# Optimization experiments

Hardware: AMD Instinct MI355X
Metric: run time of the kernel (lower is better)

The kernel has to match this reference:

```python
import jax, jax.numpy as jnp
import numpy as np

N = 50000      # nodes
E = 800000     # edges
G = 32         # graphs in batch
C = 10         # num_classes


def _glorot(key, shape):
    lim = float(np.sqrt(6.0 / (shape[0] + shape[1])))
    return jax.random.uniform(key, shape, jnp.float32, -lim, lim)


def setup_inputs() -> dict:
    key = jax.random.key(0)
    ks = jax.random.split(key, 10)
    norm = jax.random.normal(ks[0], (N, 3), jnp.float32)
    pos = jax.random.normal(ks[1], (N, 3), jnp.float32)
    x = jax.random.normal(ks[2], (N, 2), jnp.float32)
    edge_index = jax.random.randint(ks[3], (2, E), 0, N, dtype=jnp.int64)
    batch = jnp.sort(jax.random.randint(ks[4], (N,), 0, G, dtype=jnp.int64))
    return {
        'norm': norm, 'pos': pos, 'x': x,
        'edge_index': edge_index, 'batch': batch,
        'W1': _glorot(ks[5], (8, 64)),   'b1': jnp.zeros((64,), jnp.float32),
        'W2': _glorot(ks[6], (72, 128)), 'b2': jnp.zeros((128,), jnp.float32),
        'W3': _glorot(ks[7], (208, 256)),'b3': jnp.zeros((256,), jnp.float32),
        'Wl': _glorot(ks[8], (256, C)),  'bl': jnp.zeros((C,), jnp.float32),
    }


def gcn_conv(h, W, b, src, dst):
    # GCNConv(normalize=False), edge_weight == 1: out_i = sum_{(j->i)} (h_j @ W) + b
    m = h @ W                      # [N, F_out] dense transform first (cheaper than per-edge)
    msg = m[src]                   # gather per edge [E, F_out]
    agg = jax.ops.segment_sum(msg, dst, num_segments=N)
    return agg + b


def reference(norm, pos, x, edge_index, batch, W1, b1, W2, b2, W3, b3, Wl, bl):
    inp = jnp.concatenate([norm, pos, x], axis=1)      # [N, 8]
    src, dst = edge_index[0], edge_index[1]
    # dropout p=0.2 is identity at inference
    h1 = jax.nn.relu(gcn_conv(inp, W1, b1, src, dst))  # [N, 64]
    h = jnp.concatenate([h1, inp], axis=1)             # [N, 72]
    h2 = jax.nn.relu(gcn_conv(h, W2, b2, src, dst))    # [N, 128]
    h = jnp.concatenate([h, h2, inp], axis=1)          # [N, 208]
    h3 = jax.nn.relu(gcn_conv(h, W3, b3, src, dst))    # [N, 256]
    pooled = jax.ops.segment_max(h3, batch, num_segments=G)  # global_max_pool [G, 256]
    logits = pooled @ Wl + bl
    out = jax.nn.log_softmax(logits, axis=1)
    pred = jax.nn.softmax(out, axis=1)
    return (out, pred)
```

## Files before the change

kernel.cpp:

```cpp
#include <hip/hip_runtime.h>
#include <hip/hip_bf16.h>

#define NN 50000
#define EE 800000
#define GG 32
#define SCB 512

#define BSH 6
#define NBUK 782
#define NBLK1 256
#define EPB (EE / NBLK1)
#define MH (NBUK * NBLK1)
#define NB2 ((MH + SCB - 1) / SCB)
#define CAP2 2048

#define B_PREP ((NN + 255) / 256)
#define TOTW (64 * 32 + 128 * 96 + 256 * 224)
#define B_WTP ((TOTW + 255) / 256)

using short8 = __attribute__((ext_vector_type(8))) short;
using f32x4  = __attribute__((ext_vector_type(4))) float;

__device__ __forceinline__ ushort f2bf(float f) {
    __hip_bfloat16 hb = __float2bfloat16(f);
    return *reinterpret_cast<ushort*>(&hb);
}

__device__ __forceinline__ void acc8(uint4 v, float* a) {
    a[0] += __uint_as_float(v.x << 16); a[1] += __uint_as_float(v.x & 0xffff0000u);
    a[2] += __uint_as_float(v.y << 16); a[3] += __uint_as_float(v.y & 0xffff0000u);
    a[4] += __uint_as_float(v.z << 16); a[5] += __uint_as_float(v.z & 0xffff0000u);
    a[6] += __uint_as_float(v.w << 16); a[7] += __uint_as_float(v.w & 0xffff0000u);
}

__device__ __forceinline__ void wtp_one(const float* W, ushort* Wt, int K, int F,
                                        int KPAD, int mode, int idx) {
    int n = idx / KPAD, k = idx - n * KPAD;
    float v = 0.f;
    if (k < K) {
        int ko = k;
        if (mode == 2) ko = (k < 8) ? (k + 64) : (k - 8);
        v = W[(size_t)ko * F + n];
        if (mode == 1 && ko >= 64 && ko < 72) v += W[(size_t)(ko + 136) * F + n];
    }
    Wt[idx] = f2bf(v);
}


__global__ __launch_bounds__(256) void setup_k(
        const int* __restrict__ edst, int* __restrict__ hist,
        const float* __restrict__ nrm, const float* __restrict__ pos,
        const float* __restrict__ x, ushort* __restrict__ inpb,
        const float* __restrict__ W1, ushort* __restrict__ Wt1,
        const float* __restrict__ W2, ushort* __restrict__ Wt2,
        const float* __restrict__ W3, ushort* __restrict__ Wt3,
        float* __restrict__ pooled) {
    int blk = blockIdx.x, tid = threadIdx.x;
    if (blk < NBLK1) {
        __shared__ uint cnt[NBUK];
        for (int i = tid; i < NBUK; i += 256) cnt[i] = 0;
        __syncthreads();
        int base = blk * EPB;
        for (int i = tid; i < EPB; i += 256)
            atomicAdd(&cnt[(uint)edst[base + i] >> BSH], 1u);
        __syncthreads();
        for (int b = tid; b < NBUK; b += 256)
            hist[(size_t)b * NBLK1 + blk] = (int)cnt[b];
    } else if (blk < NBLK1 + B_PREP) {
        int i = (blk - NBLK1) * 256 + tid;
        if (i < NN) {
            float v[8];
            v[0] = nrm[i * 3]; v[1] = nrm[i * 3 + 1]; v[2] = nrm[i * 3 + 2];
            v[3] = pos[i * 3]; v[4] = pos[i * 3 + 1]; v[5] = pos[i * 3 + 2];
            v[6] = x[i * 2];   v[7] = x[i * 2 + 1];
            uint4 d;
            d.x = (uint)f2bf(v[0]) | ((uint)f2bf(v[1]) << 16);
            d.y = (uint)f2bf(v[2]) | ((uint)f2bf(v[3]) << 16);
            d.z = (uint)f2bf(v[4]) | ((uint)f2bf(v[5]) << 16);
            d.w = (uint)f2bf(v[6]) | ((uint)f2bf(v[7]) << 16);
            *reinterpret_cast<uint4*>(&inpb[(size_t)i * 8]) = d;
        }
    } else if (blk < NBLK1 + B_PREP + B_WTP) {
        int idx = (blk - NBLK1 - B_PREP) * 256 + tid;
        if (idx < 64 * 32) { wtp_one(W1, Wt1, 8, 64, 32, 0, idx); return; }
        idx -= 64 * 32;
        if (idx < 128 * 96) { wtp_one(W2, Wt2, 72, 128, 96, 2, idx); return; }
        idx -= 128 * 96;
        if (idx < 256 * 224) wtp_one(W3, Wt3, 200, 256, 224, 1, idx);
    } else {
        for (int q = tid; q < GG * 256; q += 256) pooled[q] = 0.f;
    }
}


__global__ __launch_bounds__(SCB) void scan1_k(const int* __restrict__ in,
                                               int* __restrict__ bsum, int M) {
    __shared__ int ws[SCB / 64];
    int tid = threadIdx.x, lane = tid & 63, w = tid >> 6;
    int i = blockIdx.x * SCB + tid;
    int s = (i < M) ? in[i] : 0;
    #pragma unroll
    for (int off = 32; off >= 1; off >>= 1) s += __shfl_down(s, off, 64);
    if (lane == 0) ws[w] = s;
    __syncthreads();
    if (tid == 0) {
        int t = 0;
        #pragma unroll
        for (int j = 0; j < SCB / 64; j++) t += ws[j];
        bsum[blockIdx.x] = t;
    }
}

__global__ __launch_bounds__(64) void scan2g_k(int* __restrict__ bsum, int nb) {
    int lane = threadIdx.x;
    int carry = 0;
    for (int base = 0; base < nb; base += 64) {
        int v = (base + lane < nb) ? bsum[base + lane] : 0;
        int s = v;
        #pragma unroll
        for (int off = 1; off < 64; off <<= 1) {
            int t = __shfl_up(s, off, 64);
            if (lane >= off) s += t;
        }
        if (base + lane < nb) bsum[base + lane] = carry + s - v;
        carry += __shfl(s, 63, 64);
    }
}

__global__ __launch_bounds__(SCB) void scan3g_k(const int* __restrict__ in,
                                                const int* __restrict__ bsum,
                                                int* __restrict__ out, int M) {
    __shared__ int ws[SCB / 64];
    int tid = threadIdx.x, lane = tid & 63, w = tid >> 6;
    int i = blockIdx.x * SCB + tid;
    int v = (i < M) ? in[i] : 0;
    int s = v;
    #pragma unroll
    for (int off = 1; off < 64; off <<= 1) {
        int t = __shfl_up(s, off, 64);
        if (lane >= off) s += t;
    }
    if (lane == 63) ws[w] = s;
    __syncthreads();
    if (w == 0 && lane < SCB / 64) {
        int t = ws[lane];
        #pragma unroll
        for (int off = 1; off < SCB / 64; off <<= 1) {
            int u = __shfl_up(t, off, 64);
            if (lane >= off) t += u;
        }
        ws[lane] = t;
    }
    __syncthreads();
    if (i < M) out[i] = (w ? ws[w - 1] : 0) + s - v + bsum[blockIdx.x];
}


__global__ __launch_bounds__(256) void bsort1_k(const int* __restrict__ esrc,
                                                const int* __restrict__ edst,
                                                const int* __restrict__ ofs,
                                                uint* __restrict__ packed) {
    __shared__ uint cnt[1024];
    __shared__ uint lofs0[1024];
    __shared__ uint goff[NBUK];
    __shared__ uint stage[EPB];
    __shared__ uint wsum[4];
    int tid = threadIdx.x, blk = blockIdx.x;
    int lane = tid & 63, wv = tid >> 6;

    for (int i = tid; i < 1024; i += 256) cnt[i] = 0;
    __syncthreads();
    int base = blk * EPB;
    for (int i = tid; i < EPB; i += 256)
        atomicAdd(&cnt[(uint)edst[base + i] >> BSH], 1u);
    __syncthreads();

    uint c0 = cnt[tid * 4 + 0], c1 = cnt[tid * 4 + 1];
    uint c2 = cnt[tid * 4 + 2], c3 = cnt[tid * 4 + 3];
    uint ts = c0 + c1 + c2 + c3;
    uint sc = ts;
    #pragma unroll
    for (int off = 1; off < 64; off <<= 1) {
        uint t = __shfl_up(sc, off, 64);
        if (lane >= off) sc += t;
    }
    if (lane == 63) wsum[wv] = sc;
    __syncthreads();
    uint wbase = 0;
    for (int j = 0; j < wv; j++) wbase += wsum[j];
    uint run = wbase + sc - ts;
    lofs0[tid * 4 + 0] = run;
    lofs0[tid * 4 + 1] = run + c0;
    lofs0[tid * 4 + 2] = run + c0 + c1;
    lofs0[tid * 4 + 3] = run + c0 + c1 + c2;
    cnt[tid * 4 + 0] = run;
    cnt[tid * 4 + 1] = run + c0;
    cnt[tid * 4 + 2] = run + c0 + c1;
    cnt[tid * 4 + 3] = run + c0 + c1 + c2;
    for (int b = tid; b < NBUK; b += 256)
        goff[b] = (uint)ofs[(size_t)b * NBLK1 + blk];
    __syncthreads();

    for (int i = tid; i < EPB; i += 256) {
        int d = edst[base + i];
        uint b = (uint)d >> BSH;
        uint pos = atomicAdd(&cnt[b], 1u);
        stage[pos] = (b << 22) | ((uint)(d & 63) << 16) | (uint)esrc[base + i];
    }
    __syncthreads();

    for (int i = tid; i < EPB; i += 256) {
        uint p = stage[i];
        uint b = p >> 22;
        packed[goff[b] + ((uint)i - lofs0[b])] = p & 0x3FFFFFu;
    }
}


__global__ __launch_bounds__(256) void bsort2_k(const uint* __restrict__ packed,
                                                const int* __restrict__ ofs,
                                                ushort* __restrict__ col,
                                                int* __restrict__ rowptr) {
    __shared__ uint buf[CAP2];
    __shared__ ushort srt[CAP2];
    __shared__ uint fcnt[64], fofs[64];
    int b = blockIdx.x, tid = threadIdx.x;
    uint g0 = (uint)ofs[(size_t)b * NBLK1];
    uint g1 = (b + 1 < NBUK) ? (uint)ofs[(size_t)(b + 1) * NBLK1] : (uint)EE;
    uint n = g1 - g0;
    if (tid < 64) fcnt[tid] = 0;
    __syncthreads();
    for (uint i = tid; i < n; i += 256) {
        uint p = packed[g0 + i];
        buf[i] = p;
        atomicAdd(&fcnt[(p >> 16) & 63], 1u);
    }
    __syncthreads();
    if (tid < 64) {
        uint v = fcnt[tid], s = v;
        #pragma unroll
        for (int off = 1; off < 64; off <<= 1) {
            uint t = __shfl_up(s, off, 64);
            if (tid >= off) s += t;
        }
        uint e0 = s - v;
        fofs[tid] = e0;
        int node = (b << BSH) + tid;
        if (node < NN) rowptr[node] = (int)(g0 + e0);
    }
    if (b == NBUK - 1 && tid == 0) rowptr[NN] = EE;
    __syncthreads();
    for (uint i = tid; i < n; i += 256) {
        uint p = buf[i];
        uint pos = atomicAdd(&fofs[(p >> 16) & 63], 1u);
        srt[pos] = (ushort)(p & 0xFFFFu);
    }
    __syncthreads();
    for (uint i = tid; i < n; i += 256) col[g0 + i] = srt[i];
}


template <int K, int KPAD, int LDA, int F, int WPA, int WPB, int WG, bool POOL>
__global__ __launch_bounds__(512) void layer_k(
        const ushort* __restrict__ preA, const ushort* __restrict__ preB,
        const ushort* __restrict__ gsrc,
        const int* __restrict__ rowptr, const ushort* __restrict__ col,
        const ushort* __restrict__ Wt, const float* __restrict__ bias,
        ushort* __restrict__ aggout, ushort* __restrict__ out,
        const int* __restrict__ batch, float* __restrict__ pooled, int N) {
    constexpr int WPRE = WPA + WPB;
    constexpr int NU4 = WG / 8;
    constexpr int TPN = (NU4 < 8) ? NU4 : 8;
    constexpr int U4PT = NU4 / TPN;
    constexpr int KS = KPAD / 32;
    constexpr int FW = F / 4;
    constexpr int NT = FW / 16;

    __shared__ ushort At[64 * LDA];
    __shared__ int batchv[64];

    const int node0 = blockIdx.x * 64;
    const int tid = threadIdx.x;
    const int lane = tid & 63;
    const int wv = tid >> 6;
    const int wm = wv & 1;
    const int wn = wv >> 1;

    {
        int m = tid / TPN;
        int j = tid - m * TPN;
        if (m < 64) {
            int i = node0 + m;
            float ga0[U4PT * 8], ga1[U4PT * 8];
            #pragma unroll
            for (int q = 0; q < U4PT * 8; q++) { ga0[q] = 0.f; ga1[q] = 0.f; }
            if (i < N) {
                int e0 = rowptr[i], e1 = rowptr[i + 1];
                int e = e0;
                for (; e + 1 < e1; e += 2) {
                    int s0 = col[e], s1 = col[e + 1];
                    #pragma unroll
                    for (int u = 0; u < U4PT; u++) {
                        uint4 v0 = *reinterpret_cast<const uint4*>(
                            &gsrc[(size_t)s0 * WG + (j * U4PT + u) * 8]);
                        uint4 v1 = *reinterpret_cast<const uint4*>(
                            &gsrc[(size_t)s1 * WG + (j * U4PT + u) * 8]);
                        acc8(v0, ga0 + u * 8);
                        acc8(v1, ga1 + u * 8);
                    }
                }
                if (e < e1) {
                    int s0 = col[e];
                    #pragma unroll
                    for (int u = 0; u < U4PT; u++) {
                        uint4 v0 = *reinterpret_cast<const uint4*>(
                            &gsrc[(size_t)s0 * WG + (j * U4PT + u) * 8]);
                        acc8(v0, ga0 + u * 8);
                    }
                }
            }
            #pragma unroll
            for (int u = 0; u < U4PT; u++) {
                uint4 o;
                o.x = (uint)f2bf(ga0[u*8+0] + ga1[u*8+0]) | ((uint)f2bf(ga0[u*8+1] + ga1[u*8+1]) << 16);
                o.y = (uint)f2bf(ga0[u*8+2] + ga1[u*8+2]) | ((uint)f2bf(ga0[u*8+3] + ga1[u*8+3]) << 16);
                o.z = (uint)f2bf(ga0[u*8+4] + ga1[u*8+4]) | ((uint)f2bf(ga0[u*8+5] + ga1[u*8+5]) << 16);
                o.w = (uint)f2bf(ga0[u*8+6] + ga1[u*8+6]) | ((uint)f2bf(ga0[u*8+7] + ga1[u*8+7]) << 16);
                *reinterpret_cast<uint4*>(&At[m * LDA + WPRE + (j * U4PT + u) * 8]) = o;
                if (aggout != nullptr && i < N)
                    *reinterpret_cast<uint4*>(&aggout[(size_t)i * WG + (j * U4PT + u) * 8]) = o;
            }
        }
        if constexpr (POOL) {
            if (tid < 64) batchv[tid] = (node0 + tid < N) ? batch[node0 + tid] : -1;
        }
    }

    if constexpr (WPRE > 0) {
        constexpr int NP = WPRE / 8;
        for (int idx = tid; idx < 64 * NP; idx += 512) {
            int m = idx / NP, q = idx - m * NP;
            int i = node0 + m;
            uint4 v = make_uint4(0, 0, 0, 0);
            if (i < N) {
                int c = q * 8;
                if (c < WPA) v = *reinterpret_cast<const uint4*>(&preA[(size_t)i * WPA + c]);
                else v = *reinterpret_cast<const uint4*>(&preB[(size_t)i * WPB + (c - WPA)]);
            }
            *reinterpret_cast<uint4*>(&At[m * LDA + q * 8]) = v;
        }
    }
    {
        constexpr int PADU4 = (KPAD - K) / 8;
        for (int idx = tid; idx < 64 * PADU4; idx += 512) {
            int m = idx / PADU4, q = idx - m * PADU4;
            *reinterpret_cast<uint4*>(&At[m * LDA + K + q * 8]) = make_uint4(0, 0, 0, 0);
        }
    }
    __syncthreads();

    const int r15 = lane & 15, kg = lane >> 4;

    short8 a[2][KS];
    #pragma unroll
    for (int s = 0; s < 2; s++)
        #pragma unroll
        for (int kc = 0; kc < KS; kc++)
            a[s][kc] = *reinterpret_cast<const short8*>(
                &At[(wm * 32 + s * 16 + r15) * LDA + kg * 8 + kc * 32]);

    f32x4 acc[2][NT];
    #pragma unroll
    for (int s = 0; s < 2; s++)
        #pragma unroll
        for (int nt = 0; nt < NT; nt++) acc[s][nt] = (f32x4){0.f, 0.f, 0.f, 0.f};

    const ushort* wbase = &Wt[(size_t)(wn * FW + r15) * KPAD + kg * 8];
    #pragma unroll
    for (int nt = 0; nt < NT; nt++) {
        short8 b[KS];
        #pragma unroll
        for (int kc = 0; kc < KS; kc++)
            b[kc] = *reinterpret_cast<const short8*>(
                wbase + (size_t)nt * 16 * KPAD + kc * 32);
        #pragma unroll
        for (int kc = 0; kc < KS; kc++) {
            acc[0][nt] = __builtin_amdgcn_mfma_f32_16x16x32_bf16(a[0][kc], b[kc], acc[0][nt], 0, 0, 0);
            acc[1][nt] = __builtin_amdgcn_mfma_f32_16x16x32_bf16(a[1][kc], b[kc], acc[1][nt], 0, 0, 0);
        }
    }

    if constexpr (!POOL) {
        #pragma unroll
        for (int s = 0; s < 2; s++)
            #pragma unroll
            for (int nt = 0; nt < NT; nt++) {
                int colg = wn * FW + nt * 16 + r15;
                float bv = bias[colg];
                #pragma unroll
                for (int reg = 0; reg < 4; reg++) {
                    int row = node0 + wm * 32 + s * 16 + kg * 4 + reg;
                    if (row < N) {
                        float v = fmaxf(acc[s][nt][reg] + bv, 0.f);
                        out[(size_t)row * F + colg] = f2bf(v);
                    }
                }
            }
    } else {
        __syncthreads();
        ushort* H3 = At;
        #pragma unroll
        for (int s = 0; s < 2; s++)
            #pragma unroll
            for (int nt = 0; nt < NT; nt++) {
                int colg = wn * FW + nt * 16 + r15;
                float bv = bias[colg];
                #pragma unroll
                for (int reg = 0; reg < 4; reg++) {
                    int m = wm * 32 + s * 16 + kg * 4 + reg;
                    float v = fmaxf(acc[s][nt][reg] + bv, 0.f);
                    H3[m * 256 + colg] = f2bf(v);
                }
            }
        __syncthreads();
        int nvalid = min(64, N - node0);
        int c = tid & 255, half = tid >> 8;
        int m0 = half * 32;
        int m1 = min(m0 + 32, nvalid);
        int curg = -1;
        float cm = 0.f;
        for (int m = m0; m < m1; m++) {
            int g = batchv[m];
            if (g != curg) {
                if (curg >= 0)
                    atomicMax(reinterpret_cast<int*>(&pooled[curg * 256 + c]),
                              __float_as_int(cm));
                curg = g;
                cm = 0.f;
            }
            cm = fmaxf(cm, __uint_as_float((uint)H3[m * 256 + c] << 16));
        }
        if (curg >= 0)
            atomicMax(reinterpret_cast<int*>(&pooled[curg * 256 + c]),
                      __float_as_int(cm));
    }
}


__global__ __launch_bounds__(320) void head_k(const float* __restrict__ pooled,
                                              const float* __restrict__ Wl,
                                              const float* __restrict__ bl,
                                              float* __restrict__ out) {
    __shared__ float lg[GG][10];
    __shared__ float lse[GG];
    int t = threadIdx.x;
    int g = t / 10, c = t % 10;
    float acc = bl[c];
    for (int k = 0; k < 256; k++) acc = fmaf(pooled[g * 256 + k], Wl[k * 10 + c], acc);
    lg[g][c] = acc;
    __syncthreads();
    if (c == 0) {
        float mx = -1e30f;
        for (int j = 0; j < 10; j++) mx = fmaxf(mx, lg[g][j]);
        float s = 0.f;
        for (int j = 0; j < 10; j++) s += expf(lg[g][j] - mx);
        lse[g] = mx + logf(s);
    }
    __syncthreads();
    float o = acc - lse[g];
    out[g * 10 + c] = o;
    out[320 + g * 10 + c] = expf(o);
}


extern "C" void kernel_launch(void* const* d_in, const int* in_sizes, int n_in,
                              void* d_out, int out_size, void* d_ws, size_t ws_size,
                              hipStream_t stream) {
    const int N = NN, E = EE;
    const float* nrm = (const float*)d_in[0];
    const float* pos = (const float*)d_in[1];
    const float* x   = (const float*)d_in[2];
    const int* ei    = (const int*)d_in[3];
    const int* batch = (const int*)d_in[4];
    const float* W1 = (const float*)d_in[5];
    const float* b1 = (const float*)d_in[6];
    const float* W2 = (const float*)d_in[7];
    const float* b2 = (const float*)d_in[8];
    const float* W3 = (const float*)d_in[9];
    const float* b3 = (const float*)d_in[10];
    const float* Wl = (const float*)d_in[11];
    const float* bl = (const float*)d_in[12];

    const int* esrc = ei;
    const int* edst = ei + E;

    char* w = (char*)d_ws;
    auto carve = [&](size_t bytes) {
        void* p = (void*)w;
        w += (bytes + 255) & ~(size_t)255;
        return p;
    };
    int* hist     = (int*)carve((size_t)MH * 4);
    int* ofs      = (int*)carve((size_t)MH * 4);
    int* bsum     = (int*)carve((size_t)NB2 * 4);
    uint* packed  = (uint*)carve((size_t)E * 4);
    int* rowptr   = (int*)carve((size_t)(N + 1) * 4);
    ushort* col   = (ushort*)carve((size_t)E * 2);
    ushort* inpb  = (ushort*)carve((size_t)N * 8 * 2);
    ushort* agg1  = (ushort*)carve((size_t)N * 8 * 2);
    ushort* h1    = (ushort*)carve((size_t)N * 64 * 2);
    ushort* aggh1 = (ushort*)carve((size_t)N * 64 * 2);
    ushort* h2    = (ushort*)carve((size_t)N * 128 * 2);
    ushort* Wt1   = (ushort*)carve((size_t)64 * 32 * 2);
    ushort* Wt2   = (ushort*)carve((size_t)128 * 96 * 2);
    ushort* Wt3   = (ushort*)carve((size_t)256 * 224 * 2);
    float* pooled = (float*)carve((size_t)GG * 256 * 4);

    setup_k<<<NBLK1 + B_PREP + B_WTP + 1, 256, 0, stream>>>(
        edst, hist, nrm, pos, x, inpb, W1, Wt1, W2, Wt2, W3, Wt3, pooled);

    scan1_k<<<NB2, SCB, 0, stream>>>(hist, bsum, MH);
    scan2g_k<<<1, 64, 0, stream>>>(bsum, NB2);
    scan3g_k<<<NB2, SCB, 0, stream>>>(hist, bsum, ofs, MH);
    bsort1_k<<<NBLK1, 256, 0, stream>>>(esrc, edst, ofs, packed);
    bsort2_k<<<NBUK, 256, 0, stream>>>(packed, ofs, col, rowptr);

    layer_k<8, 32, 40, 64, 0, 0, 8, false><<<NBUK, 512, 0, stream>>>(
        nullptr, nullptr, inpb, rowptr, col, Wt1, b1, agg1, h1, nullptr, nullptr, N);

    layer_k<72, 96, 104, 128, 8, 0, 64, false><<<NBUK, 512, 0, stream>>>(
        agg1, nullptr, h1, rowptr, col, Wt2, b2, aggh1, h2, nullptr, nullptr, N);

    layer_k<200, 224, 264, 256, 64, 8, 128, true><<<NBUK, 512, 0, stream>>>(
        aggh1, agg1, h2, rowptr, col, Wt3, b3, nullptr, nullptr, batch, pooled, N);

    head_k<<<1, 320, 0, stream>>>(pooled, Wl, bl, (float*)d_out);
}
```

Before: 138.6 us.

## Balance edge aggregation across block threads with shared-memory atomic accumulation

```diff
diff --git a/kernel.cpp b/kernel.cpp
--- a/kernel.cpp
+++ b/kernel.cpp
@@ -33,15 +33,22 @@
     a[6] += __uint_as_float(v.w << 16); a[7] += __uint_as_float(v.w & 0xffff0000u);
 }
 
+__device__ __forceinline__ short8 pack_bf8(const float* p) {
+    union { ushort u[8]; short8 s; } r;
+    #pragma unroll
+    for (int q = 0; q < 8; q++) r.u[q] = f2bf(p[q]);
+    return r.s;
+}
+
 __device__ __forceinline__ void wtp_one(const float* W, ushort* Wt, int K, int F,
                                         int KPAD, int mode, int idx) {
     int n = idx / KPAD, k = idx - n * KPAD;
     float v = 0.f;
     if (k < K) {
         int ko = k;
-        if (mode == 2) ko = (k < 8) ? (k + 64) : (k - 8);
+        if (mode == 3) ko = (k < 128) ? (k + 72) : (k - 128);
         v = W[(size_t)ko * F + n];
-        if (mode == 1 && ko >= 64 && ko < 72) v += W[(size_t)(ko + 136) * F + n];
+        if (mode == 3 && ko >= 64 && ko < 72) v += W[(size_t)(ko + 136) * F + n];
     }
     Wt[idx] = f2bf(v);
 }
@@ -84,9 +91,9 @@
         int idx = (blk - NBLK1 - B_PREP) * 256 + tid;
         if (idx < 64 * 32) { wtp_one(W1, Wt1, 8, 64, 32, 0, idx); return; }
         idx -= 64 * 32;
-        if (idx < 128 * 96) { wtp_one(W2, Wt2, 72, 128, 96, 2, idx); return; }
+        if (idx < 128 * 96) { wtp_one(W2, Wt2, 72, 128, 96, 0, idx); return; }
         idx -= 128 * 96;
-        if (idx < 256 * 224) wtp_one(W3, Wt3, 200, 256, 224, 1, idx);
+        if (idx < 256 * 224) wtp_one(W3, Wt3, 200, 256, 224, 3, idx);
     } else {
         for (int q = tid; q < GG * 256; q += 256) pooled[q] = 0.f;
     }
@@ -260,7 +267,7 @@
 }
 
 
-template <int K, int KPAD, int LDA, int F, int WPA, int WPB, int WG, bool POOL>
+template <int KPAD, int GR, int WG, int PREW, int WPA, int WPB, int F, bool POOL>
 __global__ __launch_bounds__(512) void layer_k(
         const ushort* __restrict__ preA, const ushort* __restrict__ preB,
         const ushort* __restrict__ gsrc,
@@ -268,15 +275,17 @@
         const ushort* __restrict__ Wt, const float* __restrict__ bias,
         ushort* __restrict__ aggout, ushort* __restrict__ out,
         const int* __restrict__ batch, float* __restrict__ pooled, int N) {
-    constexpr int WPRE = WPA + WPB;
-    constexpr int NU4 = WG / 8;
-    constexpr int TPN = (NU4 < 8) ? NU4 : 8;
-    constexpr int U4PT = NU4 / TPN;
-    constexpr int KS = KPAD / 32;
-    constexpr int FW = F / 4;
-    constexpr int NT = FW / 16;
-
-    __shared__ ushort At[64 * LDA];
+    constexpr int GRP = GR + 4;
+    constexpr int SL  = WG / 8;
+    constexpr int R   = 512 / SL;
+    constexpr int PRS = (PREW > 0) ? PREW + 8 : 8;
+    constexpr int KS  = KPAD / 32;
+    constexpr int FW  = F / 4;
+    constexpr int NT  = FW / 16;
+
+    __shared__ float accA[64 * GRP];
+    __shared__ ushort Atpre[(PREW > 0) ? 64 * PRS : 8];
+    __shared__ int rp[65];
     __shared__ int batchv[64];
 
     const int node0 = blockIdx.x * 64;
@@ -286,58 +295,14 @@
     const int wm = wv & 1;
     const int wn = wv >> 1;
 
-    {
-        int m = tid / TPN;
-        int j = tid - m * TPN;
-        if (m < 64) {
-            int i = node0 + m;
-            float ga0[U4PT * 8], ga1[U4PT * 8];
-            #pragma unroll
-            for (int q = 0; q < U4PT * 8; q++) { ga0[q] = 0.f; ga1[q] = 0.f; }
-            if (i < N) {
-                int e0 = rowptr[i], e1 = rowptr[i + 1];
-                int e = e0;
-                for (; e + 1 < e1; e += 2) {
-                    int s0 = col[e], s1 = col[e + 1];
-                    #pragma unroll
-                    for (int u = 0; u < U4PT; u++) {
-                        uint4 v0 = *reinterpret_cast<const uint4*>(
-                            &gsrc[(size_t)s0 * WG + (j * U4PT + u) * 8]);
-                        uint4 v1 = *reinterpret_cast<const uint4*>(
-                            &gsrc[(size_t)s1 * WG + (j * U4PT + u) * 8]);
-                        acc8(v0, ga0 + u * 8);
-                        acc8(v1, ga1 + u * 8);
-                    }
-                }
-                if (e < e1) {
-                    int s0 = col[e];
-                    #pragma unroll
-                    for (int u = 0; u < U4PT; u++) {
-                        uint4 v0 = *reinterpret_cast<const uint4*>(
-                            &gsrc[(size_t)s0 * WG + (j * U4PT + u) * 8]);
-                        acc8(v0, ga0 + u * 8);
-                    }
-                }
-            }
-            #pragma unroll
-            for (int u = 0; u < U4PT; u++) {
-                uint4 o;
-                o.x = (uint)f2bf(ga0[u*8+0] + ga1[u*8+0]) | ((uint)f2bf(ga0[u*8+1] + ga1[u*8+1]) << 16);
-                o.y = (uint)f2bf(ga0[u*8+2] + ga1[u*8+2]) | ((uint)f2bf(ga0[u*8+3] + ga1[u*8+3]) << 16);
-                o.z = (uint)f2bf(ga0[u*8+4] + ga1[u*8+4]) | ((uint)f2bf(ga0[u*8+5] + ga1[u*8+5]) << 16);
-                o.w = (uint)f2bf(ga0[u*8+6] + ga1[u*8+6]) | ((uint)f2bf(ga0[u*8+7] + ga1[u*8+7]) << 16);
-                *reinterpret_cast<uint4*>(&At[m * LDA + WPRE + (j * U4PT + u) * 8]) = o;
-                if (aggout != nullptr && i < N)
-                    *reinterpret_cast<uint4*>(&aggout[(size_t)i * WG + (j * U4PT + u) * 8]) = o;
-            }
-        }
-        if constexpr (POOL) {
-            if (tid < 64) batchv[tid] = (node0 + tid < N) ? batch[node0 + tid] : -1;
-        }
-    }
-
-    if constexpr (WPRE > 0) {
-        constexpr int NP = WPRE / 8;
+    for (int idx = tid; idx < 64 * GRP / 4; idx += 512)
+        *reinterpret_cast<float4*>(&accA[idx * 4]) = make_float4(0.f, 0.f, 0.f, 0.f);
+    if (tid < 65) rp[tid] = rowptr[min(node0 + tid, NN)];
+    if constexpr (POOL) {
+        if (tid < 64) batchv[tid] = (node0 + tid < N) ? batch[node0 + tid] : -1;
+    }
+    if constexpr (PREW > 0) {
+        constexpr int NP = PREW / 8;
         for (int idx = tid; idx < 64 * NP; idx += 512) {
             int m = idx / NP, q = idx - m * NP;
             int i = node0 + m;
@@ -345,29 +310,90 @@
             if (i < N) {
                 int c = q * 8;
                 if (c < WPA) v = *reinterpret_cast<const uint4*>(&preA[(size_t)i * WPA + c]);
-                else v = *reinterpret_cast<const uint4*>(&preB[(size_t)i * WPB + (c - WPA)]);
-            }
-            *reinterpret_cast<uint4*>(&At[m * LDA + q * 8]) = v;
-        }
-    }
+                else if (c < WPA + WPB) v = *reinterpret_cast<const uint4*>(&preB[(size_t)i * WPB + (c - WPA)]);
+            }
+            *reinterpret_cast<uint4*>(&Atpre[m * PRS + q * 8]) = v;
+        }
+    }
+    __syncthreads();
+
     {
-        constexpr int PADU4 = (KPAD - K) / 8;
-        for (int idx = tid; idx < 64 * PADU4; idx += 512) {
-            int m = idx / PADU4, q = idx - m * PADU4;
-            *reinterpret_cast<uint4*>(&At[m * LDA + K + q * 8]) = make_uint4(0, 0, 0, 0);
-        }
-    }
-    __syncthreads();
+        int e0 = rp[0], e1 = rp[64];
+        int nE = e1 - e0;
+        int j = tid % SL;
+        int r = tid / SL;
+        int per = (nE + R - 1) / R;
+        int es = e0 + r * per;
+        int ee = min(es + per, e1);
+        if (es < ee) {
+            int lo = 0, hi = 63;
+            while (lo < hi) {
+                int mid = (lo + hi + 1) >> 1;
+                if (rp[mid] <= es) lo = mid; else hi = mid - 1;
+            }
+            int m = lo;
+            float a0[8] = {0,0,0,0,0,0,0,0};
+            float a1[8] = {0,0,0,0,0,0,0,0};
+            int e = es;
+            while (true) {
+                int segend = min(rp[m + 1], ee);
+                for (; e + 1 < segend; e += 2) {
+                    int s0 = col[e], s1 = col[e + 1];
+                    uint4 v0 = *reinterpret_cast<const uint4*>(&gsrc[(size_t)s0 * WG + j * 8]);
+                    uint4 v1 = *reinterpret_cast<const uint4*>(&gsrc[(size_t)s1 * WG + j * 8]);
+                    acc8(v0, a0); acc8(v1, a1);
+                }
+                if (e < segend) {
+                    uint4 v0 = *reinterpret_cast<const uint4*>(&gsrc[(size_t)col[e] * WG + j * 8]);
+                    acc8(v0, a0); e++;
+                }
+                float* dst = &accA[m * GRP + j * 8];
+                #pragma unroll
+                for (int q = 0; q < 8; q++) atomicAdd(&dst[q], a0[q] + a1[q]);
+                if (segend >= ee) break;
+                m++;
+                while (rp[m + 1] <= e) m++;
+                #pragma unroll
+                for (int q = 0; q < 8; q++) { a0[q] = 0.f; a1[q] = 0.f; }
+            }
+        }
+    }
+    __syncthreads();
+
+    if (aggout != nullptr) {
+        constexpr int NV = WG / 8;
+        for (int idx = tid; idx < 64 * NV; idx += 512) {
+            int m = idx / NV, q = idx - m * NV;
+            int i = node0 + m;
+            if (i < N) {
+                const float* p = &accA[m * GRP + q * 8];
+                uint4 o;
+                o.x = (uint)f2bf(p[0]) | ((uint)f2bf(p[1]) << 16);
+                o.y = (uint)f2bf(p[2]) | ((uint)f2bf(p[3]) << 16);
+                o.z = (uint)f2bf(p[4]) | ((uint)f2bf(p[5]) << 16);
+                o.w = (uint)f2bf(p[6]) | ((uint)f2bf(p[7]) << 16);
+                *reinterpret_cast<uint4*>(&aggout[(size_t)i * WG + q * 8]) = o;
+            }
+        }
+    }
 
     const int r15 = lane & 15, kg = lane >> 4;
 
     short8 a[2][KS];
     #pragma unroll
-    for (int s = 0; s < 2; s++)
-        #pragma unroll
-        for (int kc = 0; kc < KS; kc++)
-            a[s][kc] = *reinterpret_cast<const short8*>(
-                &At[(wm * 32 + s * 16 + r15) * LDA + kg * 8 + kc * 32]);
+    for (int s = 0; s < 2; s++) {
+        int row = wm * 32 + s * 16 + r15;
+        #pragma unroll
+        for (int kc = 0; kc < KS; kc++) {
+            if (kc * 32 < GR) {
+                const float* p = &accA[row * GRP + kc * 32 + kg * 8];
+                a[s][kc] = pack_bf8(p);
+            } else {
+                a[s][kc] = *reinterpret_cast<const short8*>(
+                    &Atpre[row * PRS + (kc * 32 - GR) + kg * 8]);
+            }
+        }
+    }
 
     f32x4 acc[2][NT];
     #pragma unroll
@@ -408,7 +434,7 @@
             }
     } else {
         __syncthreads();
-        ushort* H3 = At;
+        ushort* H3 = reinterpret_cast<ushort*>(accA);
         #pragma unroll
         for (int s = 0; s < 2; s++)
             #pragma unroll
@@ -525,13 +551,13 @@
     bsort1_k<<<NBLK1, 256, 0, stream>>>(esrc, edst, ofs, packed);
     bsort2_k<<<NBUK, 256, 0, stream>>>(packed, ofs, col, rowptr);
 
-    layer_k<8, 32, 40, 64, 0, 0, 8, false><<<NBUK, 512, 0, stream>>>(
+    layer_k<32, 32, 8, 0, 0, 0, 64, false><<<NBUK, 512, 0, stream>>>(
         nullptr, nullptr, inpb, rowptr, col, Wt1, b1, agg1, h1, nullptr, nullptr, N);
 
-    layer_k<72, 96, 104, 128, 8, 0, 64, false><<<NBUK, 512, 0, stream>>>(
+    layer_k<96, 64, 64, 32, 8, 0, 128, false><<<NBUK, 512, 0, stream>>>(
         agg1, nullptr, h1, rowptr, col, Wt2, b2, aggh1, h2, nullptr, nullptr, N);
 
-    layer_k<200, 224, 264, 256, 64, 8, 128, true><<<NBUK, 512, 0, stream>>>(
+    layer_k<224, 128, 128, 96, 64, 8, 256, true><<<NBUK, 512, 0, stream>>>(
         aggh1, agg1, h2, rowptr, col, Wt3, b3, nullptr, nullptr, batch, pooled, N);
 
     head_k<<<1, 320, 0, stream>>>(pooled, Wl, bl, (float*)d_out);
```

New measurement: 241.8 us. +74.5%, slower.

## Template node tile size; use 32-node blocks in layer 3 with 4-way edge unroll

Applied to the files above, without the earlier changes.

```diff
diff --git a/kernel.cpp b/kernel.cpp
--- a/kernel.cpp
+++ b/kernel.cpp
@@ -13,6 +13,7 @@
 #define MH (NBUK * NBLK1)
 #define NB2 ((MH + SCB - 1) / SCB)
 #define CAP2 2048
+#define NBLK32 1563
 
 #define B_PREP ((NN + 255) / 256)
 #define TOTW (64 * 32 + 128 * 96 + 256 * 224)
@@ -260,7 +261,7 @@
 }
 
 
-template <int K, int KPAD, int LDA, int F, int WPA, int WPB, int WG, bool POOL>
+template <int NODES, int K, int KPAD, int LDA, int F, int WPA, int WPB, int WG, bool POOL>
 __global__ __launch_bounds__(512) void layer_k(
         const ushort* __restrict__ preA, const ushort* __restrict__ preB,
         const ushort* __restrict__ gsrc,
@@ -270,16 +271,17 @@
         const int* __restrict__ batch, float* __restrict__ pooled, int N) {
     constexpr int WPRE = WPA + WPB;
     constexpr int NU4 = WG / 8;
-    constexpr int TPN = (NU4 < 8) ? NU4 : 8;
-    constexpr int U4PT = NU4 / TPN;
+    constexpr int TPN = (NU4 * NODES >= 512) ? (512 / NODES) : NU4;
+    static_assert(NU4 / TPN == 1, "one uint4 slice per thread");
     constexpr int KS = KPAD / 32;
     constexpr int FW = F / 4;
     constexpr int NT = FW / 16;
-
-    __shared__ ushort At[64 * LDA];
-    __shared__ int batchv[64];
-
-    const int node0 = blockIdx.x * 64;
+    constexpr int SM = NODES / 32;
+
+    __shared__ ushort At[NODES * LDA];
+    __shared__ int batchv[NODES];
+
+    const int node0 = blockIdx.x * NODES;
     const int tid = threadIdx.x;
     const int lane = tid & 63;
     const int wv = tid >> 6;
@@ -289,56 +291,45 @@
     {
         int m = tid / TPN;
         int j = tid - m * TPN;
-        if (m < 64) {
+        if (m < NODES) {
             int i = node0 + m;
-            float ga0[U4PT * 8], ga1[U4PT * 8];
-            #pragma unroll
-            for (int q = 0; q < U4PT * 8; q++) { ga0[q] = 0.f; ga1[q] = 0.f; }
+            float a0[8] = {0,0,0,0,0,0,0,0};
+            float a1[8] = {0,0,0,0,0,0,0,0};
+            float a2[8] = {0,0,0,0,0,0,0,0};
+            float a3[8] = {0,0,0,0,0,0,0,0};
             if (i < N) {
                 int e0 = rowptr[i], e1 = rowptr[i + 1];
                 int e = e0;
-                for (; e + 1 < e1; e += 2) {
-                    int s0 = col[e], s1 = col[e + 1];
-                    #pragma unroll
-                    for (int u = 0; u < U4PT; u++) {
-                        uint4 v0 = *reinterpret_cast<const uint4*>(
-                            &gsrc[(size_t)s0 * WG + (j * U4PT + u) * 8]);
-                        uint4 v1 = *reinterpret_cast<const uint4*>(
-                            &gsrc[(size_t)s1 * WG + (j * U4PT + u) * 8]);
-                        acc8(v0, ga0 + u * 8);
-                        acc8(v1, ga1 + u * 8);
-                    }
+                for (; e + 3 < e1; e += 4) {
+                    int s0 = col[e], s1 = col[e + 1], s2 = col[e + 2], s3 = col[e + 3];
+                    uint4 v0 = *reinterpret_cast<const uint4*>(&gsrc[(size_t)s0 * WG + j * 8]);
+                    uint4 v1 = *reinterpret_cast<const uint4*>(&gsrc[(size_t)s1 * WG + j * 8]);
+                    uint4 v2 = *reinterpret_cast<const uint4*>(&gsrc[(size_t)s2 * WG + j * 8]);
+                    uint4 v3 = *reinterpret_cast<const uint4*>(&gsrc[(size_t)s3 * WG + j * 8]);
+                    acc8(v0, a0); acc8(v1, a1); acc8(v2, a2); acc8(v3, a3);
                 }
-                if (e < e1) {
-                    int s0 = col[e];
-                    #pragma unroll
-                    for (int u = 0; u < U4PT; u++) {
-                        uint4 v0 = *reinterpret_cast<const uint4*>(
-                            &gsrc[(size_t)s0 * WG + (j * U4PT + u) * 8]);
-                        acc8(v0, ga0 + u * 8);
-                    }
+                for (; e < e1; e++) {
+                    uint4 v0 = *reinterpret_cast<const uint4*>(&gsrc[(size_t)col[e] * WG + j * 8]);
+                    acc8(v0, a0);
                 }
             }
-            #pragma unroll
-            for (int u = 0; u < U4PT; u++) {
-                uint4 o;
-                o.x = (uint)f2bf(ga0[u*8+0] + ga1[u*8+0]) | ((uint)f2bf(ga0[u*8+1] + ga1[u*8+1]) << 16);
-                o.y = (uint)f2bf(ga0[u*8+2] + ga1[u*8+2]) | ((uint)f2bf(ga0[u*8+3] + ga1[u*8+3]) << 16);
-                o.z = (uint)f2bf(ga0[u*8+4] + ga1[u*8+4]) | ((uint)f2bf(ga0[u*8+5] + ga1[u*8+5]) << 16);
-                o.w = (uint)f2bf(ga0[u*8+6] + ga1[u*8+6]) | ((uint)f2bf(ga0[u*8+7] + ga1[u*8+7]) << 16);
-                *reinterpret_cast<uint4*>(&At[m * LDA + WPRE + (j * U4PT + u) * 8]) = o;
-                if (aggout != nullptr && i < N)
-                    *reinterpret_cast<uint4*>(&aggout[(size_t)i * WG + (j * U4PT + u) * 8]) = o;
-            }
+            uint4 o;
+            o.x = (uint)f2bf((a0[0]+a1[0])+(a2[0]+a3[0])) | ((uint)f2bf((a0[1]+a1[1])+(a2[1]+a3[1])) << 16);
+            o.y = (uint)f2bf((a0[2]+a1[2])+(a2[2]+a3[2])) | ((uint)f2bf((a0[3]+a1[3])+(a2[3]+a3[3])) << 16);
+            o.z = (uint)f2bf((a0[4]+a1[4])+(a2[4]+a3[4])) | ((uint)f2bf((a0[5]+a1[5])+(a2[5]+a3[5])) << 16);
+            o.w = (uint)f2bf((a0[6]+a1[6])+(a2[6]+a3[6])) | ((uint)f2bf((a0[7]+a1[7])+(a2[7]+a3[7])) << 16);
+            *reinterpret_cast<uint4*>(&At[m * LDA + WPRE + j * 8]) = o;
+            if (aggout != nullptr && i < N)
+                *reinterpret_cast<uint4*>(&aggout[(size_t)i * WG + j * 8]) = o;
         }
         if constexpr (POOL) {
-            if (tid < 64) batchv[tid] = (node0 + tid < N) ? batch[node0 + tid] : -1;
+            if (tid < NODES) batchv[tid] = (node0 + tid < N) ? batch[node0 + tid] : -1;
         }
     }
 
     if constexpr (WPRE > 0) {
         constexpr int NP = WPRE / 8;
-        for (int idx = tid; idx < 64 * NP; idx += 512) {
+        for (int idx = tid; idx < NODES * NP; idx += 512) {
             int m = idx / NP, q = idx - m * NP;
             int i = node0 + m;
             uint4 v = make_uint4(0, 0, 0, 0);
@@ -351,27 +342,27 @@
         }
     }
     {
-        constexpr int PADU4 = (KPAD - K) / 8;
-        for (int idx = tid; idx < 64 * PADU4; idx += 512) {
-            int m = idx / PADU4, q = idx - m * PADU4;
-            *reinterpret_cast<uint4*>(&At[m * LDA + K + q * 8]) = make_uint4(0, 0, 0, 0);
+        constexpr int PAD = LDA - K;
+        for (int idx = tid; idx < NODES * PAD; idx += 512) {
+            int m = idx / PAD, k = K + (idx - m * PAD);
+            At[m * LDA + k] = 0;
         }
     }
     __syncthreads();
 
     const int r15 = lane & 15, kg = lane >> 4;
 
-    short8 a[2][KS];
+    short8 a[SM][KS];
     #pragma unroll
-    for (int s = 0; s < 2; s++)
+    for (int s = 0; s < SM; s++)
         #pragma unroll
         for (int kc = 0; kc < KS; kc++)
             a[s][kc] = *reinterpret_cast<const short8*>(
-                &At[(wm * 32 + s * 16 + r15) * LDA + kg * 8 + kc * 32]);
-
-    f32x4 acc[2][NT];
+                &At[(wm * (NODES / 2) + s * 16 + r15) * LDA + kg * 8 + kc * 32]);
+
+    f32x4 acc[SM][NT];
     #pragma unroll
-    for (int s = 0; s < 2; s++)
+    for (int s = 0; s < SM; s++)
         #pragma unroll
         for (int nt = 0; nt < NT; nt++) acc[s][nt] = (f32x4){0.f, 0.f, 0.f, 0.f};
 
@@ -384,22 +375,22 @@
             b[kc] = *reinterpret_cast<const short8*>(
                 wbase + (size_t)nt * 16 * KPAD + kc * 32);
         #pragma unroll
-        for (int kc = 0; kc < KS; kc++) {
-            acc[0][nt] = __builtin_amdgcn_mfma_f32_16x16x32_bf16(a[0][kc], b[kc], acc[0][nt], 0, 0, 0);
-            acc[1][nt] = __builtin_amdgcn_mfma_f32_16x16x32_bf16(a[1][kc], b[kc], acc[1][nt], 0, 0, 0);
-        }
+        for (int kc = 0; kc < KS; kc++)
+            #pragma unroll
+            for (int s = 0; s < SM; s++)
+                acc[s][nt] = __builtin_amdgcn_mfma_f32_16x16x32_bf16(a[s][kc], b[kc], acc[s][nt], 0, 0, 0);
     }
 
     if constexpr (!POOL) {
         #pragma unroll
-        for (int s = 0; s < 2; s++)
+        for (int s = 0; s < SM; s++)
             #pragma unroll
             for (int nt = 0; nt < NT; nt++) {
                 int colg = wn * FW + nt * 16 + r15;
                 float bv = bias[colg];
                 #pragma unroll
                 for (int reg = 0; reg < 4; reg++) {
-                    int row = node0 + wm * 32 + s * 16 + kg * 4 + reg;
+                    int row = node0 + wm * (NODES / 2) + s * 16 + kg * 4 + reg;
                     if (row < N) {
                         float v = fmaxf(acc[s][nt][reg] + bv, 0.f);
                         out[(size_t)row * F + colg] = f2bf(v);
@@ -410,23 +401,23 @@
         __syncthreads();
         ushort* H3 = At;
         #pragma unroll
-        for (int s = 0; s < 2; s++)
+        for (int s = 0; s < SM; s++)
             #pragma unroll
             for (int nt = 0; nt < NT; nt++) {
                 int colg = wn * FW + nt * 16 + r15;
                 float bv = bias[colg];
                 #pragma unroll
                 for (int reg = 0; reg < 4; reg++) {
-                    int m = wm * 32 + s * 16 + kg * 4 + reg;
+                    int m = wm * (NODES / 2) + s * 16 + kg * 4 + reg;
                     float v = fmaxf(acc[s][nt][reg] + bv, 0.f);
                     H3[m * 256 + colg] = f2bf(v);
                 }
             }
         __syncthreads();
-        int nvalid = min(64, N - node0);
+        int nvalid = min(NODES, N - node0);
         int c = tid & 255, half = tid >> 8;
-        int m0 = half * 32;
-        int m1 = min(m0 + 32, nvalid);
+        int m0 = half * (NODES / 2);
+        int m1 = min(m0 + NODES / 2, nvalid);
         int curg = -1;
         float cm = 0.f;
         for (int m = m0; m < m1; m++) {
@@ -525,13 +516,13 @@
     bsort1_k<<<NBLK1, 256, 0, stream>>>(esrc, edst, ofs, packed);
     bsort2_k<<<NBUK, 256, 0, stream>>>(packed, ofs, col, rowptr);
 
-    layer_k<8, 32, 40, 64, 0, 0, 8, false><<<NBUK, 512, 0, stream>>>(
+    layer_k<64, 8, 32, 40, 64, 0, 0, 8, false><<<NBUK, 512, 0, stream>>>(
         nullptr, nullptr, inpb, rowptr, col, Wt1, b1, agg1, h1, nullptr, nullptr, N);
 
-    layer_k<72, 96, 104, 128, 8, 0, 64, false><<<NBUK, 512, 0, stream>>>(
+    layer_k<64, 72, 96, 104, 128, 8, 0, 64, false><<<NBUK, 512, 0, stream>>>(
         agg1, nullptr, h1, rowptr, col, Wt2, b2, aggh1, h2, nullptr, nullptr, N);
 
-    layer_k<200, 224, 264, 256, 64, 8, 128, true><<<NBUK, 512, 0, stream>>>(
+    layer_k<32, 200, 224, 264, 256, 64, 8, 128, true><<<NBLK32, 512, 0, stream>>>(
         aggh1, agg1, h2, rowptr, col, Wt3, b3, nullptr, nullptr, batch, pooled, N);
 
     head_k<<<1, 320, 0, stream>>>(pooled, Wl, bl, (float*)d_out);
```

Measured after the change: 154.9 us. +11.8%, slower.

## Split layer-3 aggregation into sliced gather kernel with feature-sliced h2 layout

Applied to the files above, without the earlier changes.

```diff
diff --git a/kernel.cpp b/kernel.cpp
--- a/kernel.cpp
+++ b/kernel.cpp
@@ -13,6 +13,10 @@
 #define MH (NBUK * NBLK1)
 #define NB2 ((MH + SCB - 1) / SCB)
 #define CAP2 2048
+
+#define NSL 8
+#define CHN 256
+#define NCH ((NN + CHN - 1) / CHN)
 
 #define B_PREP ((NN + 255) / 256)
 #define TOTW (64 * 32 + 128 * 96 + 256 * 224)
@@ -260,24 +264,23 @@
 }
 
 
-template <int K, int KPAD, int LDA, int F, int WPA, int WPB, int WG, bool POOL>
+template <int K, int KPAD, int LDA, int F, int WPA, int WPB, int WG, bool SLICEOUT>
 __global__ __launch_bounds__(512) void layer_k(
         const ushort* __restrict__ preA, const ushort* __restrict__ preB,
         const ushort* __restrict__ gsrc,
         const int* __restrict__ rowptr, const ushort* __restrict__ col,
         const ushort* __restrict__ Wt, const float* __restrict__ bias,
-        ushort* __restrict__ aggout, ushort* __restrict__ out,
-        const int* __restrict__ batch, float* __restrict__ pooled, int N) {
+        ushort* __restrict__ aggout, ushort* __restrict__ out, int N) {
     constexpr int WPRE = WPA + WPB;
     constexpr int NU4 = WG / 8;
     constexpr int TPN = (NU4 < 8) ? NU4 : 8;
+    static_assert(NU4 / TPN >= 1, "");
     constexpr int U4PT = NU4 / TPN;
     constexpr int KS = KPAD / 32;
     constexpr int FW = F / 4;
     constexpr int NT = FW / 16;
 
     __shared__ ushort At[64 * LDA];
-    __shared__ int batchv[64];
 
     const int node0 = blockIdx.x * 64;
     const int tid = threadIdx.x;
@@ -331,9 +334,6 @@
                     *reinterpret_cast<uint4*>(&aggout[(size_t)i * WG + (j * U4PT + u) * 8]) = o;
             }
         }
-        if constexpr (POOL) {
-            if (tid < 64) batchv[tid] = (node0 + tid < N) ? batch[node0 + tid] : -1;
-        }
     }
 
     if constexpr (WPRE > 0) {
@@ -351,10 +351,10 @@
         }
     }
     {
-        constexpr int PADU4 = (KPAD - K) / 8;
-        for (int idx = tid; idx < 64 * PADU4; idx += 512) {
-            int m = idx / PADU4, q = idx - m * PADU4;
-            *reinterpret_cast<uint4*>(&At[m * LDA + K + q * 8]) = make_uint4(0, 0, 0, 0);
+        constexpr int PAD = LDA - K;
+        for (int idx = tid; idx < 64 * PAD; idx += 512) {
+            int m = idx / PAD, k = K + (idx - m * PAD);
+            At[m * LDA + k] = 0;
         }
     }
     __syncthreads();
@@ -390,60 +390,181 @@
         }
     }
 
-    if constexpr (!POOL) {
-        #pragma unroll
-        for (int s = 0; s < 2; s++)
+    #pragma unroll
+    for (int s = 0; s < 2; s++)
+        #pragma unroll
+        for (int nt = 0; nt < NT; nt++) {
+            int colg = wn * FW + nt * 16 + r15;
+            float bv = bias[colg];
             #pragma unroll
-            for (int nt = 0; nt < NT; nt++) {
-                int colg = wn * FW + nt * 16 + r15;
-                float bv = bias[colg];
-                #pragma unroll
-                for (int reg = 0; reg < 4; reg++) {
-                    int row = node0 + wm * 32 + s * 16 + kg * 4 + reg;
-                    if (row < N) {
-                        float v = fmaxf(acc[s][nt][reg] + bv, 0.f);
+            for (int reg = 0; reg < 4; reg++) {
+                int row = node0 + wm * 32 + s * 16 + kg * 4 + reg;
+                if (row < N) {
+                    float v = fmaxf(acc[s][nt][reg] + bv, 0.f);
+                    if constexpr (SLICEOUT)
+                        out[((size_t)(colg >> 4) * NN + row) * 16 + (colg & 15)] = f2bf(v);
+                    else
                         out[(size_t)row * F + colg] = f2bf(v);
-                    }
                 }
             }
-    } else {
-        __syncthreads();
-        ushort* H3 = At;
-        #pragma unroll
-        for (int s = 0; s < 2; s++)
+        }
+}
+
+
+__global__ __launch_bounds__(512) void agg3s_k(const int* __restrict__ rowptr,
+                                               const ushort* __restrict__ col,
+                                               const ushort* __restrict__ h2s,
+                                               ushort* __restrict__ aggh2s, int N) {
+    int slice = blockIdx.x % NSL;
+    int chunk = blockIdx.x / NSL;
+    int m = chunk * CHN + (threadIdx.x >> 1);
+    int h = threadIdx.x & 1;
+    if (m >= N) return;
+    const ushort* src = h2s + ((size_t)slice * NN) * 16 + h * 8;
+    float a0[8] = {0,0,0,0,0,0,0,0};
+    float a1[8] = {0,0,0,0,0,0,0,0};
+    float a2[8] = {0,0,0,0,0,0,0,0};
+    float a3[8] = {0,0,0,0,0,0,0,0};
+    int e0 = rowptr[m], e1 = rowptr[m + 1];
+    int e = e0;
+    for (; e + 3 < e1; e += 4) {
+        int s0 = col[e], s1 = col[e + 1], s2 = col[e + 2], s3 = col[e + 3];
+        uint4 v0 = *reinterpret_cast<const uint4*>(&src[(size_t)s0 * 16]);
+        uint4 v1 = *reinterpret_cast<const uint4*>(&src[(size_t)s1 * 16]);
+        uint4 v2 = *reinterpret_cast<const uint4*>(&src[(size_t)s2 * 16]);
+        uint4 v3 = *reinterpret_cast<const uint4*>(&src[(size_t)s3 * 16]);
+        acc8(v0, a0); acc8(v1, a1); acc8(v2, a2); acc8(v3, a3);
+    }
+    for (; e < e1; e++) {
+        uint4 v0 = *reinterpret_cast<const uint4*>(&src[(size_t)col[e] * 16]);
+        acc8(v0, a0);
+    }
+    uint4 o;
+    o.x = (uint)f2bf((a0[0]+a1[0])+(a2[0]+a3[0])) | ((uint)f2bf((a0[1]+a1[1])+(a2[1]+a3[1])) << 16);
+    o.y = (uint)f2bf((a0[2]+a1[2])+(a2[2]+a3[2])) | ((uint)f2bf((a0[3]+a1[3])+(a2[3]+a3[3])) << 16);
+    o.z = (uint)f2bf((a0[4]+a1[4])+(a2[4]+a3[4])) | ((uint)f2bf((a0[5]+a1[5])+(a2[5]+a3[5])) << 16);
+    o.w = (uint)f2bf((a0[6]+a1[6])+(a2[6]+a3[6])) | ((uint)f2bf((a0[7]+a1[7])+(a2[7]+a3[7])) << 16);
+    *reinterpret_cast<uint4*>(&aggh2s[((size_t)slice * NN + m) * 16 + h * 8]) = o;
+}
+
+
+__global__ __launch_bounds__(512) void layer3_k(
+        const ushort* __restrict__ aggh1, const ushort* __restrict__ agg1,
+        const ushort* __restrict__ aggh2s,
+        const ushort* __restrict__ Wt, const float* __restrict__ bias,
+        const int* __restrict__ batch, float* __restrict__ pooled, int N) {
+    constexpr int KPAD = 224, LDA = 264, F = 256;
+    constexpr int KS = KPAD / 32;
+    constexpr int FW = F / 4;
+    constexpr int NT = FW / 16;
+
+    __shared__ ushort At[64 * LDA];
+    __shared__ int batchv[64];
+
+    const int node0 = blockIdx.x * 64;
+    const int tid = threadIdx.x;
+    const int lane = tid & 63;
+    const int wv = tid >> 6;
+    const int wm = wv & 1;
+    const int wn = wv >> 1;
+
+    for (int idx = tid; idx < 64 * 8; idx += 512) {
+        int m = idx >> 3, q = idx & 7;
+        int i = node0 + m;
+        uint4 v = make_uint4(0, 0, 0, 0);
+        if (i < N) v = *reinterpret_cast<const uint4*>(&aggh1[(size_t)i * 64 + q * 8]);
+        *reinterpret_cast<uint4*>(&At[m * LDA + q * 8]) = v;
+    }
+    for (int idx = tid; idx < 64; idx += 512) {
+        int m = idx;
+        int i = node0 + m;
+        uint4 v = make_uint4(0, 0, 0, 0);
+        if (i < N) v = *reinterpret_cast<const uint4*>(&agg1[(size_t)i * 8]);
+        *reinterpret_cast<uint4*>(&At[m * LDA + 64]) = v;
+    }
+    for (int idx = tid; idx < 64 * 16; idx += 512) {
+        int m = idx >> 4;
+        int s = (idx >> 1) & 7, h = idx & 1;
+        int i = node0 + m;
+        uint4 v = make_uint4(0, 0, 0, 0);
+        if (i < N) v = *reinterpret_cast<const uint4*>(
+            &aggh2s[((size_t)s * NN + i) * 16 + h * 8]);
+        *reinterpret_cast<uint4*>(&At[m * LDA + 72 + s * 16 + h * 8]) = v;
+    }
+    for (int idx = tid; idx < 64 * 3; idx += 512) {
+        int m = idx / 3, q = idx - m * 3;
+        *reinterpret_cast<uint4*>(&At[m * LDA + 200 + q * 8]) = make_uint4(0, 0, 0, 0);
+    }
+    if (tid < 64) batchv[tid] = (node0 + tid < N) ? batch[node0 + tid] : -1;
+    __syncthreads();
+
+    const int r15 = lane & 15, kg = lane >> 4;
+
+    short8 a[2][KS];
+    #pragma unroll
+    for (int s = 0; s < 2; s++)
+        #pragma unroll
+        for (int kc = 0; kc < KS; kc++)
+            a[s][kc] = *reinterpret_cast<const short8*>(
+                &At[(wm * 32 + s * 16 + r15) * LDA + kg * 8 + kc * 32]);
+
+    f32x4 acc[2][NT];
+    #pragma unroll
+    for (int s = 0; s < 2; s++)
+        #pragma unroll
+        for (int nt = 0; nt < NT; nt++) acc[s][nt] = (f32x4){0.f, 0.f, 0.f, 0.f};
+
+    const ushort* wbase = &Wt[(size_t)(wn * FW + r15) * KPAD + kg * 8];
+    #pragma unroll
+    for (int nt = 0; nt < NT; nt++) {
+        short8 b[KS];
+        #pragma unroll
+        for (int kc = 0; kc < KS; kc++)
+            b[kc] = *reinterpret_cast<const short8*>(
+                wbase + (size_t)nt * 16 * KPAD + kc * 32);
+        #pragma unroll
+        for (int kc = 0; kc < KS; kc++) {
+            acc[0][nt] = __builtin_amdgcn_mfma_f32_16x16x32_bf16(a[0][kc], b[kc], acc[0][nt], 0, 0, 0);
+            acc[1][nt] = __builtin_amdgcn_mfma_f32_16x16x32_bf16(a[1][kc], b[kc], acc[1][nt], 0, 0, 0);
+        }
+    }
+
+    __syncthreads();
+    ushort* H3 = At;
+    #pragma unroll
+    for (int s = 0; s < 2; s++)
+        #pragma unroll
+        for (int nt = 0; nt < NT; nt++) {
+            int colg = wn * FW + nt * 16 + r15;
+            float bv = bias[colg];
             #pragma unroll
-            for (int nt = 0; nt < NT; nt++) {
-                int colg = wn * FW + nt * 16 + r15;
-                float bv = bias[colg];
-                #pragma unroll
-                for (int reg = 0; reg < 4; reg++) {
-                    int m = wm * 32 + s * 16 + kg * 4 + reg;
-                    float v = fmaxf(acc[s][nt][reg] + bv, 0.f);
-                    H3[m * 256 + colg] = f2bf(v);
-                }
+            for (int reg = 0; reg < 4; reg++) {
+                int m = wm * 32 + s * 16 + kg * 4 + reg;
+                float v = fmaxf(acc[s][nt][reg] + bv, 0.f);
+                H3[m * 256 + colg] = f2bf(v);
             }
-        __syncthreads();
-        int nvalid = min(64, N - node0);
-        int c = tid & 255, half = tid >> 8;
-        int m0 = half * 32;
-        int m1 = min(m0 + 32, nvalid);
-        int curg = -1;
-        float cm = 0.f;
-        for (int m = m0; m < m1; m++) {
-            int g = batchv[m];
-            if (g != curg) {
-                if (curg >= 0)
-                    atomicMax(reinterpret_cast<int*>(&pooled[curg * 256 + c]),
-                              __float_as_int(cm));
-                curg = g;
-                cm = 0.f;
-            }
-            cm = fmaxf(cm, __uint_as_float((uint)H3[m * 256 + c] << 16));
-        }
-        if (curg >= 0)
-            atomicMax(reinterpret_cast<int*>(&pooled[curg * 256 + c]),
-                      __float_as_int(cm));
-    }
+        }
+    __syncthreads();
+    int nvalid = min(64, N - node0);
+    int c = tid & 255, half = tid >> 8;
+    int m0 = half * 32;
+    int m1 = min(m0 + 32, nvalid);
+    int curg = -1;
+    float cm = 0.f;
+    for (int m = m0; m < m1; m++) {
+        int g = batchv[m];
+        if (g != curg) {
+            if (curg >= 0)
+                atomicMax(reinterpret_cast<int*>(&pooled[curg * 256 + c]),
+                          __float_as_int(cm));
+            curg = g;
+            cm = 0.f;
+        }
+        cm = fmaxf(cm, __uint_as_float((uint)H3[m * 256 + c] << 16));
+    }
+    if (curg >= 0)
+        atomicMax(reinterpret_cast<int*>(&pooled[curg * 256 + c]),
+                  __float_as_int(cm));
 }
 
 
@@ -510,7 +631,8 @@
     ushort* agg1  = (ushort*)carve((size_t)N * 8 * 2);
     ushort* h1    = (ushort*)carve((size_t)N * 64 * 2);
     ushort* aggh1 = (ushort*)carve((size_t)N * 64 * 2);
-    ushort* h2    = (ushort*)carve((size_t)N * 128 * 2);
+    ushort* h2s   = (ushort*)carve((size_t)NSL * N * 16 * 2);
+    ushort* aggh2s= (ushort*)carve((size_t)NSL * N * 16 * 2);
     ushort* Wt1   = (ushort*)carve((size_t)64 * 32 * 2);
     ushort* Wt2   = (ushort*)carve((size_t)128 * 96 * 2);
     ushort* Wt3   = (ushort*)carve((size_t)256 * 224 * 2);
@@ -526,13 +648,14 @@
     bsort2_k<<<NBUK, 256, 0, stream>>>(packed, ofs, col, rowptr);
 
     layer_k<8, 32, 40, 64, 0, 0, 8, false><<<NBUK, 512, 0, stream>>>(
-        nullptr, nullptr, inpb, rowptr, col, Wt1, b1, agg1, h1, nullptr, nullptr, N);
-
-    layer_k<72, 96, 104, 128, 8, 0, 64, false><<<NBUK, 512, 0, stream>>>(
-        agg1, nullptr, h1, rowptr, col, Wt2, b2, aggh1, h2, nullptr, nullptr, N);
-
-    layer_k<200, 224, 264, 256, 64, 8, 128, true><<<NBUK, 512, 0, stream>>>(
-        aggh1, agg1, h2, rowptr, col, Wt3, b3, nullptr, nullptr, batch, pooled, N);
+        nullptr, nullptr, inpb, rowptr, col, Wt1, b1, agg1, h1, N);
+
+    layer_k<72, 96, 104, 128, 8, 0, 64, true><<<NBUK, 512, 0, stream>>>(
+        agg1, nullptr, h1, rowptr, col, Wt2, b2, aggh1, h2s, N);
+
+    agg3s_k<<<NCH * NSL, 512, 0, stream>>>(rowptr, col, h2s, aggh2s, N);
+
+    layer3_k<<<NBUK, 512, 0, stream>>>(aggh1, agg1, aggh2s, Wt3, b3, batch, pooled, N);
 
     head_k<<<1, 320, 0, stream>>>(pooled, Wl, bl, (float*)d_out);
 }
```

After: 149.5 us. 7.9% more time.
